# Optimization experiments

Measured on AMD Instinct MI355X. Metric: run time of the kernel, lower is better.

The kernel has to match this reference:

```python
import jax, jax.numpy as jnp
import numpy as np
import math

Q, WAY, SHOT, M, D = 50, 5, 5, 196, 640
N_ITERS = 5
VAR_FLOOR = 0.01

def _inv_softplus(v):
    return math.log(math.expm1(v))

def setup_inputs() -> dict:
    key = jax.random.key(0)
    k1, k2, k3 = jax.random.split(key, 3)
    # L2-normalized tokens so cost = 1 - cosine sim is well-scaled
    q = jax.random.normal(k1, (Q, M, D), dtype=jnp.float32)
    q = q / jnp.linalg.norm(q, axis=-1, keepdims=True)
    s = jax.random.normal(k2, (WAY, SHOT, M, D), dtype=jnp.float32)
    s = s / jnp.linalg.norm(s, axis=-1, keepdims=True)
    var = jax.random.uniform(k3, (WAY, D), dtype=jnp.float32, minval=0.5, maxval=1.5)
    eps_raw = jnp.asarray(_inv_softplus(0.1), dtype=jnp.float32)           # eps_init=0.1
    tau_local_raw = jnp.asarray(_inv_softplus(1.0 - 0.01), dtype=jnp.float32)  # tau_local_init=1.0
    return {"query_tokens": q, "support_tokens": s, "variance": var,
            "eps_raw": eps_raw, "tau_local_raw": tau_local_raw}

def reference(query_tokens, support_tokens, variance, eps_raw, tau_local_raw):
    eps = jax.nn.softplus(eps_raw) + 1e-4
    tau = jax.nn.softplus(tau_local_raw) + 0.01
    way, shot, m, d = support_tokens.shape
    km = shot * m
    nq = query_tokens.shape[0]
    # dimension weights from variance (use_vhat_coupling=True)
    w = 1.0 / (variance + VAR_FLOOR)                              # [way, d]
    w = w / jnp.maximum(w.sum(axis=-1, keepdims=True), 1e-6) * d
    support_weighted = support_tokens.reshape(way, km, d) * w[:, None, :]
    sim = jnp.einsum('qmd,wkd->qwmk', query_tokens, support_weighted)  # [q, way, m, km]
    cost = 1.0 - sim
    log_K = -cost / eps
    log_mu = jnp.full((nq, way, m), -math.log(float(m)), dtype=log_K.dtype)
    log_nu = jnp.full((nq, way, km), -math.log(float(km)), dtype=log_K.dtype)

    def step(carry, _):
        u, v = carry
        v = log_nu - jax.nn.logsumexp(log_K + u[..., None], axis=-2)
        u = log_mu - jax.nn.logsumexp(log_K + v[..., None, :], axis=-1)
        return (u, v), None

    (u, v), _ = jax.lax.scan(step, (jnp.zeros_like(log_mu), jnp.zeros_like(log_nu)),
                             None, length=N_ITERS)
    gamma = jnp.exp(log_K + u[..., None] + v[..., None, :])
    ot_cost = jnp.sum(gamma * cost, axis=(-1, -2))                # [q, way]
    return -ot_cost / tau
```

## Files before the change

### kernel.cpp

```cpp
#include <hip/hip_runtime.h>
#include <hip/hip_bf16.h>
#include <hip/hip_fp16.h>

#define QN    50
#define NWAY  5
#define NPAIR 250
#define MM    196
#define KMM   980
#define KP    984
#define DD    640
#define NITER 5

typedef __attribute__((ext_vector_type(8)))  short short8;
typedef __attribute__((ext_vector_type(16))) float f32x16;

#define EXP2F(x) __builtin_exp2f(x)
#define RCPF(x)  __builtin_amdgcn_rcpf(x)

#define E4M3_UP 1.3292279957849159e36f
#define E4M3_DN 7.5231638452626401e-37f

__device__ __forceinline__ short bf16bits(float f) {
  __hip_bfloat16 h = __float2bfloat16(f);
  return *reinterpret_cast<short*>(&h);
}

__device__ __forceinline__ unsigned int f32_to_e4m3(float x) {
  unsigned int b = __float_as_uint(x);
  unsigned int sgn = (b >> 24) & 0x80u;
  float a = __uint_as_float(b & 0x7FFFFFFFu);
  a = fminf(a, 448.0f);
  unsigned int z = __float_as_uint(a * E4M3_DN);
  unsigned int mag = (z + 0x00080000u) >> 20;
  return sgn | mag;
}
__device__ __forceinline__ float e4m3_to_f32(unsigned int v) {
  return __uint_as_float(((v & 0x80u) << 24) | ((v & 0x7Fu) << 20)) * E4M3_UP;
}
__device__ __forceinline__ float dec8(unsigned int word, int byte) {
  return e4m3_to_f32((word >> (8 * byte)) & 0xFFu);
}

__device__ __forceinline__ void h2AtomicAdd(__half2* addr, float a, float b) {
  unsigned int* ui = reinterpret_cast<unsigned int*>(addr);
  unsigned int old = __hip_atomic_load(ui, __ATOMIC_RELAXED, __HIP_MEMORY_SCOPE_AGENT);
  unsigned int assumed;
  do {
    assumed = old;
    __half2 cur = *reinterpret_cast<__half2*>(&assumed);
    float2 cf = __half22float2(cur);
    __half2 sum = __floats2half2_rn(cf.x + a, cf.y + b);
    unsigned int ns = *reinterpret_cast<unsigned int*>(&sum);
    old = atomicCAS(ui, assumed, ns);
  } while (old != assumed);
}

__global__ __launch_bounds__(256, 3)
void gemm_kernel(const float* __restrict__ qt, const float* __restrict__ st,
                 const float* __restrict__ var, const float* __restrict__ epsr,
                 unsigned char* __restrict__ cost, __half* __restrict__ T1)
{
  __shared__ __align__(16) unsigned short Ash[128 * 64];
  __shared__ __align__(16) unsigned short Bsh[128 * 64];
  __shared__ __align__(16) float w_lds[DD];
  __shared__ float cs_lds[128];
  __shared__ float red_s;

  const int tid  = threadIdx.x;
  const int wv   = tid >> 6;
  const int lane = tid & 63;
  const int l31  = lane & 31;
  const int lh   = lane >> 5;
  const int wm   = wv >> 1;
  const int wn   = wv & 1;

  const int lg   = (blockIdx.x & 7) * 500 + (blockIdx.x >> 3);
  const int pair = lg >> 4;
  const int mt_  = (lg >> 3) & 1;
  const int nt_  = lg & 7;
  const int wi = pair / 50, qi = pair % 50;
  const int m0 = mt_ * 128, n0 = nt_ * 128;

  const float eps = logf(1.0f + expf(epsr[0])) + 1e-4f;
  const float C2  = 1.4426950408889634f / eps;

  float psum = 0.f;
  for (int d = tid; d < DD; d += 256) {
    float inv = 1.0f / (var[wi * DD + d] + 0.01f);
    w_lds[d] = inv; psum += inv;
  }
  #pragma unroll
  for (int s = 32; s; s >>= 1) psum += __shfl_xor(psum, s);
  if (tid == 0) red_s = 0.f;
  if (tid < 128) cs_lds[tid] = 0.f;
  __syncthreads();
  if (lane == 0) atomicAdd(&red_s, psum);
  __syncthreads();
  const float wsc = (float)DD / fmaxf(red_s, 1e-6f);
  for (int d = tid; d < DD; d += 256) w_lds[d] *= wsc;
  __syncthreads();

  const float* qb = qt + (size_t)qi * MM * DD;
  const float* sb = st + (size_t)wi * KMM * DD;

  f32x16 acc[2][2];
  #pragma unroll
  for (int i = 0; i < 2; ++i)
    #pragma unroll
    for (int j = 0; j < 2; ++j)
      #pragma unroll
      for (int e = 0; e < 16; ++e) acc[i][j][e] = 0.f;

  const int srow = tid >> 3;
  const int sslt = tid & 7;

  float4 ra0[4], ra1[4], rb0[4], rb1[4];
  #pragma unroll
  for (int i = 0; i < 4; ++i) {
    const int r = i * 32 + srow;
    const float* sa = qb + (size_t)min(m0 + r, MM - 1) * DD + sslt * 8;
    ra0[i] = *reinterpret_cast<const float4*>(sa);
    ra1[i] = *reinterpret_cast<const float4*>(sa + 4);
    const float* sbp = sb + (size_t)min(n0 + r, KMM - 1) * DD + sslt * 8;
    rb0[i] = *reinterpret_cast<const float4*>(sbp);
    rb1[i] = *reinterpret_cast<const float4*>(sbp + 4);
  }

  #pragma unroll
  for (int ks = 0; ks < 10; ++ks) {
    const int kd = ks * 64 + sslt * 8;
    float4 w0 = *reinterpret_cast<const float4*>(w_lds + kd);
    float4 w1 = *reinterpret_cast<const float4*>(w_lds + kd + 4);
    #pragma unroll
    for (int i = 0; i < 4; ++i) {
      const int r = i * 32 + srow;
      const int wslt = (sslt ^ (r & 7)) * 8;
      short8 pk;
      pk[0] = bf16bits(ra0[i].x); pk[1] = bf16bits(ra0[i].y);
      pk[2] = bf16bits(ra0[i].z); pk[3] = bf16bits(ra0[i].w);
      pk[4] = bf16bits(ra1[i].x); pk[5] = bf16bits(ra1[i].y);
      pk[6] = bf16bits(ra1[i].z); pk[7] = bf16bits(ra1[i].w);
      *reinterpret_cast<short8*>(&Ash[r * 64 + wslt]) = pk;
      short8 qk;
      qk[0] = bf16bits(rb0[i].x * w0.x); qk[1] = bf16bits(rb0[i].y * w0.y);
      qk[2] = bf16bits(rb0[i].z * w0.z); qk[3] = bf16bits(rb0[i].w * w0.w);
      qk[4] = bf16bits(rb1[i].x * w1.x); qk[5] = bf16bits(rb1[i].y * w1.y);
      qk[6] = bf16bits(rb1[i].z * w1.z); qk[7] = bf16bits(rb1[i].w * w1.w);
      *reinterpret_cast<short8*>(&Bsh[r * 64 + wslt]) = qk;
    }
    __syncthreads();
    if (ks < 9) {
      const int kn = (ks + 1) * 64 + sslt * 8;
      #pragma unroll
      for (int i = 0; i < 4; ++i) {
        const int r = i * 32 + srow;
        const float* sa = qb + (size_t)min(m0 + r, MM - 1) * DD + kn;
        ra0[i] = *reinterpret_cast<const float4*>(sa);
        ra1[i] = *reinterpret_cast<const float4*>(sa + 4);
        const float* sbp = sb + (size_t)min(n0 + r, KMM - 1) * DD + kn;
        rb0[i] = *reinterpret_cast<const float4*>(sbp);
        rb1[i] = *reinterpret_cast<const float4*>(sbp + 4);
      }
    }
    #pragma unroll
    for (int kk = 0; kk < 4; ++kk) {
      const int ph = ((kk * 2 + lh) ^ (l31 & 7)) * 8;
      short8 a0 = *reinterpret_cast<short8*>(&Ash[(wm * 64      + l31) * 64 + ph]);
      short8 a1 = *reinterpret_cast<short8*>(&Ash[(wm * 64 + 32 + l31) * 64 + ph]);
      short8 b0 = *reinterpret_cast<short8*>(&Bsh[(wn * 64      + l31) * 64 + ph]);
      short8 b1 = *reinterpret_cast<short8*>(&Bsh[(wn * 64 + 32 + l31) * 64 + ph]);
      acc[0][0] = __builtin_amdgcn_mfma_f32_32x32x16_bf16(a0, b0, acc[0][0], 0, 0, 0);
      acc[0][1] = __builtin_amdgcn_mfma_f32_32x32x16_bf16(a0, b1, acc[0][1], 0, 0, 0);
      acc[1][0] = __builtin_amdgcn_mfma_f32_32x32x16_bf16(a1, b0, acc[1][0], 0, 0, 0);
      acc[1][1] = __builtin_amdgcn_mfma_f32_32x32x16_bf16(a1, b1, acc[1][1], 0, 0, 0);
    }
    __syncthreads();
  }

  unsigned char* cb = cost + (size_t)pair * (MM * KP);
  #pragma unroll
  for (int nt = 0; nt < 2; ++nt) {
    const int ncol = n0 + wn * 64 + nt * 32 + l31;
    float part = 0.f;
    #pragma unroll
    for (int mt = 0; mt < 2; ++mt) {
      #pragma unroll
      for (int r = 0; r < 16; ++r) {
        const int mrow = m0 + wm * 64 + mt * 32 + (r & 3) + 8 * (r >> 2) + 4 * lh;
        if (mrow < MM && ncol < KMM) {
          unsigned int enc = f32_to_e4m3(acc[mt][nt][r] * C2);
          cb[(size_t)mrow * KP + ncol] = (unsigned char)enc;
          part += EXP2F(e4m3_to_f32(enc));
        }
      }
    }
    atomicAdd(&cs_lds[wn * 64 + nt * 32 + l31], part);
  }
  __syncthreads();
  if (tid < 64) {
    const int c0 = n0 + 2 * tid;
    if (c0 < KMM)
      h2AtomicAdd(reinterpret_cast<__half2*>(T1 + (size_t)pair * KMM + c0),
                  cs_lds[2 * tid], cs_lds[2 * tid + 1]);
  }
}

template<bool FIN>
__global__ __launch_bounds__(256)
void sweep_kernel(const unsigned char* __restrict__ cost, const __half* __restrict__ Tin,
                  __half* __restrict__ Tout, const float* __restrict__ epsr,
                  const float* __restrict__ taur, float* __restrict__ outp)
{
  __shared__ float part[4][1024];
  const int tid  = threadIdx.x;
  const int wave = tid >> 6;
  const int lane = tid & 63;
  const int pair   = blockIdx.x / 7;
  const int mchunk = blockIdx.x % 7;

  const unsigned char* cb = cost + (size_t)pair * (MM * KP);
  const __half* tp = Tin + (size_t)pair * KMM;

  const int k1 = 8 * lane;
  const int k2 = 512 + 8 * lane;

  float iT[16];
  {
    uint2 ta = *reinterpret_cast<const uint2*>(tp + k1);
    uint2 tb = *reinterpret_cast<const uint2*>(tp + k1 + 4);
    uint2 tc = *reinterpret_cast<const uint2*>(tp + k2);
    uint2 td = *reinterpret_cast<const uint2*>(tp + k2 + 4);
    float2 f;
    f = __half22float2(*reinterpret_cast<const __half2*>(&ta.x)); iT[0] = RCPF(980.f * f.x); iT[1] = RCPF(980.f * f.y);
    f = __half22float2(*reinterpret_cast<const __half2*>(&ta.y)); iT[2] = RCPF(980.f * f.x); iT[3] = RCPF(980.f * f.y);
    f = __half22float2(*reinterpret_cast<const __half2*>(&tb.x)); iT[4] = RCPF(980.f * f.x); iT[5] = RCPF(980.f * f.y);
    f = __half22float2(*reinterpret_cast<const __half2*>(&tb.y)); iT[6] = RCPF(980.f * f.x); iT[7] = RCPF(980.f * f.y);
    f = __half22float2(*reinterpret_cast<const __half2*>(&tc.x)); iT[8] = RCPF(980.f * f.x); iT[9] = RCPF(980.f * f.y);
    f = __half22float2(*reinterpret_cast<const __half2*>(&tc.y)); iT[10] = RCPF(980.f * f.x); iT[11] = RCPF(980.f * f.y);
    f = __half22float2(*reinterpret_cast<const __half2*>(&td.x)); iT[12] = RCPF(980.f * f.x); iT[13] = RCPF(980.f * f.y);
    f = __half22float2(*reinterpret_cast<const __half2*>(&td.y)); iT[14] = RCPF(980.f * f.x); iT[15] = RCPF(980.f * f.y);
    #pragma unroll
    for (int e = 8; e < 16; ++e)
      if (k2 + (e - 8) >= KMM) iT[e] = 0.f;
  }

  float acc[16];
  #pragma unroll
  for (int e = 0; e < 16; ++e) acc[e] = 0.f;

  float scal = 0.f, c2f = 0.f, rowtot = 0.f;
  if (FIN) {
    const float eps = logf(1.0f + expf(epsr[0])) + 1e-4f;
    c2f = 1.4426950408889634f / eps;
    const float tau = logf(1.0f + expf(taur[0])) + 0.01f;
    scal = 1.0f / (tau * c2f);
  }

  #pragma unroll
  for (int r = 0; r < 7; ++r) {
    const int m = mchunk * 28 + wave * 7 + r;
    const unsigned char* rp = cb + (size_t)m * KP;
    uint2 w1 = *reinterpret_cast<const uint2*>(rp + k1);
    uint2 w2 = *reinterpret_cast<const uint2*>(rp + k2);
    float r_[16], p_[16];
    #pragma unroll
    for (int e = 0; e < 4; ++e) {
      r_[e]      = dec8(w1.x, e);
      r_[4 + e]  = dec8(w1.y, e);
      r_[8 + e]  = dec8(w2.x, e);
      r_[12 + e] = dec8(w2.y, e);
    }
    #pragma unroll
    for (int e = 0; e < 16; ++e) p_[e] = EXP2F(r_[e]);
    #pragma unroll
    for (int e = 8; e < 16; ++e)
      if (k2 + (e - 8) >= KMM) p_[e] = 0.f;

    float A = 0.f, Bv = 0.f;
    #pragma unroll
    for (int e = 0; e < 16; ++e) {
      float ee = p_[e] * iT[e];
      A += ee;
      if (FIN) Bv += ee * r_[e];
    }
    #pragma unroll
    for (int s = 32; s; s >>= 1) {
      A += __shfl_xor(A, s);
      if (FIN) Bv += __shfl_xor(Bv, s);
    }
    const float up = RCPF(196.0f * A);
    if (FIN) {
      rowtot += Bv * up - c2f * (1.0f / 196.0f);
    } else {
      #pragma unroll
      for (int e = 0; e < 16; ++e) acc[e] += p_[e] * up;
    }
  }

  if (FIN) {
    if (lane == 0) {
      const int opair = (pair % 50) * NWAY + (pair / 50);
      atomicAdd(outp + opair, rowtot * scal);
    }
  } else {
    #pragma unroll
    for (int e = 0; e < 8; ++e) part[wave][k1 + e] = acc[e];
    #pragma unroll
    for (int e = 0; e < 8; ++e) part[wave][k2 + e] = acc[8 + e];
    __syncthreads();
    __half* top = Tout + (size_t)pair * KMM;
    for (int c2c = tid; c2c < KMM / 2; c2c += 256) {
      const int c = 2 * c2c;
      float s0 = part[0][c]     + part[1][c]     + part[2][c]     + part[3][c];
      float s1 = part[0][c + 1] + part[1][c + 1] + part[2][c + 1] + part[3][c + 1];
      h2AtomicAdd(reinterpret_cast<__half2*>(top + c), s0, s1);
    }
  }
}

extern "C" void kernel_launch(void* const* d_in, const int* in_sizes, int n_in,
                              void* d_out, int out_size, void* d_ws, size_t ws_size,
                              hipStream_t stream) {
  const float* qt  = (const float*)d_in[0];
  const float* st  = (const float*)d_in[1];
  const float* var = (const float*)d_in[2];
  const float* er  = (const float*)d_in[3];
  const float* tr  = (const float*)d_in[4];
  float* out = (float*)d_out;

  char* ws = (char*)d_ws;
  unsigned char* cost = (unsigned char*)ws;
  __half* Ta = (__half*)(ws + 48216000);
  __half* Tb = (__half*)(ws + 48216000 + 490000);

  (void)hipMemsetAsync(out, 0, NPAIR * sizeof(float), stream);
  (void)hipMemsetAsync(Ta, 0, (size_t)NPAIR * KMM * sizeof(__half), stream);

  gemm_kernel<<<NPAIR * 16, 256, 0, stream>>>(qt, st, var, er, cost, Ta);

  __half* cur = Ta;
  __half* nxt = Tb;
  for (int it = 0; it < NITER - 1; ++it) {
    (void)hipMemsetAsync(nxt, 0, (size_t)NPAIR * KMM * sizeof(__half), stream);
    sweep_kernel<false><<<NPAIR * 7, 256, 0, stream>>>(cost, cur, nxt, er, tr, out);
    __half* t = cur; cur = nxt; nxt = t;
  }
  sweep_kernel<true><<<NPAIR * 7, 256, 0, stream>>>(cost, cur, nullptr, er, tr, out);
}
```

Measured before the change: 392.1 us.

## Pre-convert query and weighted support tokens to bf16 before GEMM

Adds two prep kernels: one computes the normalized variance weights per way, the other converts the query tokens and the weighted support tokens to bf16 once into workspace. The GEMM kernel then loads bf16 directly, which halves global load bytes and drops the per-block weight computation and conversion work repeated across 4000 blocks. It also raises the launch-bounds occupancy hint from 3 to 4 blocks and reorders the epilogue loop. In exchange it adds two kernel launches and an extra write and read pass over about 15 MB of converted data.

Result: faster. 360.6 us (-8.0%).

```diff
diff --git a/kernel.cpp b/kernel.cpp
--- a/kernel.cpp
+++ b/kernel.cpp
@@ -37,8 +37,11 @@
 __device__ __forceinline__ float e4m3_to_f32(unsigned int v) {
   return __uint_as_float(((v & 0x80u) << 24) | ((v & 0x7Fu) << 20)) * E4M3_UP;
 }
-__device__ __forceinline__ float dec8(unsigned int word, int byte) {
-  return e4m3_to_f32((word >> (8 * byte)) & 0xFFu);
+__device__ __forceinline__ void dec4(unsigned int w, float* out) {
+  out[0] = e4m3_to_f32(w & 0xFFu);
+  out[1] = e4m3_to_f32((w >> 8) & 0xFFu);
+  out[2] = e4m3_to_f32((w >> 16) & 0xFFu);
+  out[3] = e4m3_to_f32((w >> 24) & 0xFFu);
 }
 
 __device__ __forceinline__ void h2AtomicAdd(__half2* addr, float a, float b) {
@@ -55,16 +58,67 @@
   } while (old != assumed);
 }
 
-__global__ __launch_bounds__(256, 3)
-void gemm_kernel(const float* __restrict__ qt, const float* __restrict__ st,
-                 const float* __restrict__ var, const float* __restrict__ epsr,
+__global__ __launch_bounds__(256)
+void prep_w(const float* __restrict__ var, float* __restrict__ wbuf)
+{
+  __shared__ float red[4];
+  const int way = blockIdx.x, tid = threadIdx.x;
+  float s = 0.f;
+  for (int d = tid; d < DD; d += 256) s += 1.0f / (var[way * DD + d] + 0.01f);
+  #pragma unroll
+  for (int sh = 32; sh; sh >>= 1) s += __shfl_xor(s, sh);
+  if ((tid & 63) == 0) red[tid >> 6] = s;
+  __syncthreads();
+  const float tot = red[0] + red[1] + red[2] + red[3];
+  const float sc  = (float)DD / fmaxf(tot, 1e-6f);
+  for (int d = tid; d < DD; d += 256)
+    wbuf[way * DD + d] = sc / (var[way * DD + d] + 0.01f);
+}
+
+#define QUNITS 784000
+#define TUNITS 1176000
+__global__ __launch_bounds__(256)
+void prep_cvt(const float* __restrict__ qt, const float* __restrict__ st,
+              const float* __restrict__ wbuf,
+              unsigned short* __restrict__ qb16, unsigned short* __restrict__ sw16)
+{
+  const size_t u = (size_t)blockIdx.x * 256 + threadIdx.x;
+  if (u >= TUNITS) return;
+  short8 o;
+  if (u < QUNITS) {
+    const float* src = qt + u * 8;
+    float4 f0 = *reinterpret_cast<const float4*>(src);
+    float4 f1 = *reinterpret_cast<const float4*>(src + 4);
+    o[0] = bf16bits(f0.x); o[1] = bf16bits(f0.y); o[2] = bf16bits(f0.z); o[3] = bf16bits(f0.w);
+    o[4] = bf16bits(f1.x); o[5] = bf16bits(f1.y); o[6] = bf16bits(f1.z); o[7] = bf16bits(f1.w);
+    *reinterpret_cast<short8*>(qb16 + u * 8) = o;
+  } else {
+    const size_t e = (u - QUNITS) * 8;
+    const int d0 = (int)(e % DD);
+    const int way = (int)(e / ((size_t)KMM * DD));
+    const float* src = st + e;
+    const float* wp  = wbuf + way * DD + d0;
+    float4 f0 = *reinterpret_cast<const float4*>(src);
+    float4 f1 = *reinterpret_cast<const float4*>(src + 4);
+    float4 w0 = *reinterpret_cast<const float4*>(wp);
+    float4 w1 = *reinterpret_cast<const float4*>(wp + 4);
+    o[0] = bf16bits(f0.x * w0.x); o[1] = bf16bits(f0.y * w0.y);
+    o[2] = bf16bits(f0.z * w0.z); o[3] = bf16bits(f0.w * w0.w);
+    o[4] = bf16bits(f1.x * w1.x); o[5] = bf16bits(f1.y * w1.y);
+    o[6] = bf16bits(f1.z * w1.z); o[7] = bf16bits(f1.w * w1.w);
+    *reinterpret_cast<short8*>(sw16 + e) = o;
+  }
+}
+
+__global__ __launch_bounds__(256, 4)
+void gemm_kernel(const unsigned short* __restrict__ qb16,
+                 const unsigned short* __restrict__ sw16,
+                 const float* __restrict__ epsr,
                  unsigned char* __restrict__ cost, __half* __restrict__ T1)
 {
   __shared__ __align__(16) unsigned short Ash[128 * 64];
   __shared__ __align__(16) unsigned short Bsh[128 * 64];
-  __shared__ __align__(16) float w_lds[DD];
   __shared__ float cs_lds[128];
-  __shared__ float red_s;
 
   const int tid  = threadIdx.x;
   const int wv   = tid >> 6;
@@ -84,24 +138,8 @@
   const float eps = logf(1.0f + expf(epsr[0])) + 1e-4f;
   const float C2  = 1.4426950408889634f / eps;
 
-  float psum = 0.f;
-  for (int d = tid; d < DD; d += 256) {
-    float inv = 1.0f / (var[wi * DD + d] + 0.01f);
-    w_lds[d] = inv; psum += inv;
-  }
-  #pragma unroll
-  for (int s = 32; s; s >>= 1) psum += __shfl_xor(psum, s);
-  if (tid == 0) red_s = 0.f;
-  if (tid < 128) cs_lds[tid] = 0.f;
-  __syncthreads();
-  if (lane == 0) atomicAdd(&red_s, psum);
-  __syncthreads();
-  const float wsc = (float)DD / fmaxf(red_s, 1e-6f);
-  for (int d = tid; d < DD; d += 256) w_lds[d] *= wsc;
-  __syncthreads();
-
-  const float* qb = qt + (size_t)qi * MM * DD;
-  const float* sb = st + (size_t)wi * KMM * DD;
+  const unsigned short* qb = qb16 + (size_t)qi * MM * DD;
+  const unsigned short* sb = sw16 + (size_t)wi * KMM * DD;
 
   f32x16 acc[2][2];
   #pragma unroll
@@ -114,39 +152,23 @@
   const int srow = tid >> 3;
   const int sslt = tid & 7;
 
-  float4 ra0[4], ra1[4], rb0[4], rb1[4];
+  short8 pa[4], pb[4];
   #pragma unroll
   for (int i = 0; i < 4; ++i) {
     const int r = i * 32 + srow;
-    const float* sa = qb + (size_t)min(m0 + r, MM - 1) * DD + sslt * 8;
-    ra0[i] = *reinterpret_cast<const float4*>(sa);
-    ra1[i] = *reinterpret_cast<const float4*>(sa + 4);
-    const float* sbp = sb + (size_t)min(n0 + r, KMM - 1) * DD + sslt * 8;
-    rb0[i] = *reinterpret_cast<const float4*>(sbp);
-    rb1[i] = *reinterpret_cast<const float4*>(sbp + 4);
-  }
+    pa[i] = *reinterpret_cast<const short8*>(qb + (size_t)min(m0 + r, MM - 1) * DD + sslt * 8);
+    pb[i] = *reinterpret_cast<const short8*>(sb + (size_t)min(n0 + r, KMM - 1) * DD + sslt * 8);
+  }
+  if (tid < 128) cs_lds[tid] = 0.f;
 
   #pragma unroll
   for (int ks = 0; ks < 10; ++ks) {
-    const int kd = ks * 64 + sslt * 8;
-    float4 w0 = *reinterpret_cast<const float4*>(w_lds + kd);
-    float4 w1 = *reinterpret_cast<const float4*>(w_lds + kd + 4);
     #pragma unroll
     for (int i = 0; i < 4; ++i) {
       const int r = i * 32 + srow;
       const int wslt = (sslt ^ (r & 7)) * 8;
-      short8 pk;
-      pk[0] = bf16bits(ra0[i].x); pk[1] = bf16bits(ra0[i].y);
-      pk[2] = bf16bits(ra0[i].z); pk[3] = bf16bits(ra0[i].w);
-      pk[4] = bf16bits(ra1[i].x); pk[5] = bf16bits(ra1[i].y);
-      pk[6] = bf16bits(ra1[i].z); pk[7] = bf16bits(ra1[i].w);
-      *reinterpret_cast<short8*>(&Ash[r * 64 + wslt]) = pk;
-      short8 qk;
-      qk[0] = bf16bits(rb0[i].x * w0.x); qk[1] = bf16bits(rb0[i].y * w0.y);
-      qk[2] = bf16bits(rb0[i].z * w0.z); qk[3] = bf16bits(rb0[i].w * w0.w);
-      qk[4] = bf16bits(rb1[i].x * w1.x); qk[5] = bf16bits(rb1[i].y * w1.y);
-      qk[6] = bf16bits(rb1[i].z * w1.z); qk[7] = bf16bits(rb1[i].w * w1.w);
-      *reinterpret_cast<short8*>(&Bsh[r * 64 + wslt]) = qk;
+      *reinterpret_cast<short8*>(&Ash[r * 64 + wslt]) = pa[i];
+      *reinterpret_cast<short8*>(&Bsh[r * 64 + wslt]) = pb[i];
     }
     __syncthreads();
     if (ks < 9) {
@@ -154,12 +176,8 @@
       #pragma unroll
       for (int i = 0; i < 4; ++i) {
         const int r = i * 32 + srow;
-        const float* sa = qb + (size_t)min(m0 + r, MM - 1) * DD + kn;
-        ra0[i] = *reinterpret_cast<const float4*>(sa);
-        ra1[i] = *reinterpret_cast<const float4*>(sa + 4);
-        const float* sbp = sb + (size_t)min(n0 + r, KMM - 1) * DD + kn;
-        rb0[i] = *reinterpret_cast<const float4*>(sbp);
-        rb1[i] = *reinterpret_cast<const float4*>(sbp + 4);
+        pa[i] = *reinterpret_cast<const short8*>(qb + (size_t)min(m0 + r, MM - 1) * DD + kn);
+        pb[i] = *reinterpret_cast<const short8*>(sb + (size_t)min(n0 + r, KMM - 1) * DD + kn);
       }
     }
     #pragma unroll
@@ -183,15 +201,18 @@
     const int ncol = n0 + wn * 64 + nt * 32 + l31;
     float part = 0.f;
     #pragma unroll
-    for (int mt = 0; mt < 2; ++mt) {
-      #pragma unroll
-      for (int r = 0; r < 16; ++r) {
-        const int mrow = m0 + wm * 64 + mt * 32 + (r & 3) + 8 * (r >> 2) + 4 * lh;
-        if (mrow < MM && ncol < KMM) {
-          unsigned int enc = f32_to_e4m3(acc[mt][nt][r] * C2);
-          cb[(size_t)mrow * KP + ncol] = (unsigned char)enc;
-          part += EXP2F(e4m3_to_f32(enc));
-        }
+    for (int r = 0; r < 16; ++r) {
+      const int mrow = m0 + wm * 64 + (r & 3) + 8 * (r >> 2) + 4 * lh;
+      if (mrow < MM && ncol < KMM) {
+        unsigned int enc = f32_to_e4m3(acc[0][nt][r] * C2);
+        cb[(size_t)mrow * KP + ncol] = (unsigned char)enc;
+        part += EXP2F(e4m3_to_f32(enc));
+      }
+      const int mrow2 = mrow + 32;
+      if (mrow2 < MM && ncol < KMM) {
+        unsigned int enc = f32_to_e4m3(acc[1][nt][r] * C2);
+        cb[(size_t)mrow2 * KP + ncol] = (unsigned char)enc;
+        part += EXP2F(e4m3_to_f32(enc));
       }
     }
     atomicAdd(&cs_lds[wn * 64 + nt * 32 + l31], part);
@@ -231,11 +252,11 @@
     uint2 tc = *reinterpret_cast<const uint2*>(tp + k2);
     uint2 td = *reinterpret_cast<const uint2*>(tp + k2 + 4);
     float2 f;
-    f = __half22float2(*reinterpret_cast<const __half2*>(&ta.x)); iT[0] = RCPF(980.f * f.x); iT[1] = RCPF(980.f * f.y);
-    f = __half22float2(*reinterpret_cast<const __half2*>(&ta.y)); iT[2] = RCPF(980.f * f.x); iT[3] = RCPF(980.f * f.y);
-    f = __half22float2(*reinterpret_cast<const __half2*>(&tb.x)); iT[4] = RCPF(980.f * f.x); iT[5] = RCPF(980.f * f.y);
-    f = __half22float2(*reinterpret_cast<const __half2*>(&tb.y)); iT[6] = RCPF(980.f * f.x); iT[7] = RCPF(980.f * f.y);
-    f = __half22float2(*reinterpret_cast<const __half2*>(&tc.x)); iT[8] = RCPF(980.f * f.x); iT[9] = RCPF(980.f * f.y);
+    f = __half22float2(*reinterpret_cast<const __half2*>(&ta.x)); iT[0]  = RCPF(980.f * f.x); iT[1]  = RCPF(980.f * f.y);
+    f = __half22float2(*reinterpret_cast<const __half2*>(&ta.y)); iT[2]  = RCPF(980.f * f.x); iT[3]  = RCPF(980.f * f.y);
+    f = __half22float2(*reinterpret_cast<const __half2*>(&tb.x)); iT[4]  = RCPF(980.f * f.x); iT[5]  = RCPF(980.f * f.y);
+    f = __half22float2(*reinterpret_cast<const __half2*>(&tb.y)); iT[6]  = RCPF(980.f * f.x); iT[7]  = RCPF(980.f * f.y);
+    f = __half22float2(*reinterpret_cast<const __half2*>(&tc.x)); iT[8]  = RCPF(980.f * f.x); iT[9]  = RCPF(980.f * f.y);
     f = __half22float2(*reinterpret_cast<const __half2*>(&tc.y)); iT[10] = RCPF(980.f * f.x); iT[11] = RCPF(980.f * f.y);
     f = __half22float2(*reinterpret_cast<const __half2*>(&td.x)); iT[12] = RCPF(980.f * f.x); iT[13] = RCPF(980.f * f.y);
     f = __half22float2(*reinterpret_cast<const __half2*>(&td.y)); iT[14] = RCPF(980.f * f.x); iT[15] = RCPF(980.f * f.y);
@@ -263,13 +284,8 @@
     uint2 w1 = *reinterpret_cast<const uint2*>(rp + k1);
     uint2 w2 = *reinterpret_cast<const uint2*>(rp + k2);
     float r_[16], p_[16];
-    #pragma unroll
-    for (int e = 0; e < 4; ++e) {
-      r_[e]      = dec8(w1.x, e);
-      r_[4 + e]  = dec8(w1.y, e);
-      r_[8 + e]  = dec8(w2.x, e);
-      r_[12 + e] = dec8(w2.y, e);
-    }
+    dec4(w1.x, r_ + 0);  dec4(w1.y, r_ + 4);
+    dec4(w2.x, r_ + 8);  dec4(w2.y, r_ + 12);
     #pragma unroll
     for (int e = 0; e < 16; ++e) p_[e] = EXP2F(r_[e]);
     #pragma unroll
@@ -331,12 +347,17 @@
   char* ws = (char*)d_ws;
   unsigned char* cost = (unsigned char*)ws;
   __half* Ta = (__half*)(ws + 48216000);
-  __half* Tb = (__half*)(ws + 48216000 + 490000);
+  __half* Tb = (__half*)(ws + 48706000);
+  float* wbuf = (float*)(ws + 49196000);
+  unsigned short* qb16 = (unsigned short*)(ws + 49208800);
+  unsigned short* sw16 = (unsigned short*)(ws + 61752800);
 
   (void)hipMemsetAsync(out, 0, NPAIR * sizeof(float), stream);
   (void)hipMemsetAsync(Ta, 0, (size_t)NPAIR * KMM * sizeof(__half), stream);
 
-  gemm_kernel<<<NPAIR * 16, 256, 0, stream>>>(qt, st, var, er, cost, Ta);
+  prep_w<<<NWAY, 256, 0, stream>>>(var, wbuf);
+  prep_cvt<<<(TUNITS + 255) / 256, 256, 0, stream>>>(qt, st, wbuf, qb16, sw16);
+  gemm_kernel<<<NPAIR * 16, 256, 0, stream>>>(qb16, sw16, er, cost, Ta);
 
   __half* cur = Ta;
   __half* nxt = Tb;
```
